# Performance work log

Hardware: AMD Instinct MI355X
Metric: run time of the kernel (lower is better)

## Reference

```python
import jax, jax.numpy as jnp
import numpy as np

B, S, H = 1, 2048, 4096
N_HEADS, N_KV, HEAD_DIM = 32, 8, 128
ROPE_THETA = 10000.0


def setup_inputs() -> dict:
    key = jax.random.key(0)
    k1, k2, k3 = jax.random.split(key, 3)
    hidden_states = jax.random.normal(k1, (B, S, H), dtype=jnp.float32)
    # fused QKV projection weight: rows = (n_heads + 2*n_kv_heads) * head_dim
    Wqkv = jax.random.normal(k2, ((N_HEADS + 2 * N_KV) * HEAD_DIM, H), dtype=jnp.float32) * 0.02
    Wo = jax.random.normal(k3, (H, N_HEADS * HEAD_DIM), dtype=jnp.float32) * 0.02
    return {"hidden_states": hidden_states, "Wqkv": Wqkv, "Wo": Wo}


def _rope_tables(seqlen, dim, theta):
    inv_freq = 1.0 / (theta ** (jnp.arange(0, dim, 2, dtype=jnp.float32) / dim))  # [dim/2]
    t = jnp.arange(seqlen, dtype=jnp.float32)
    freqs = jnp.outer(t, inv_freq)  # [S, dim/2]
    return jnp.cos(freqs), jnp.sin(freqs)


def _apply_rope(x, cos, sin):
    # torch code: reshape(...,2,-1).transpose -> view_as_complex pairs (x[j], x[j+d/2])
    # i.e. NeoX rotate-half on first/second halves of head_dim.
    d2 = x.shape[-1] // 2
    x1, x2 = x[..., :d2], x[..., d2:]
    c = cos[None, :, None, :]  # [1,S,1,d/2]
    s = sin[None, :, None, :]
    return jnp.concatenate([x1 * c - x2 * s, x1 * s + x2 * c], axis=-1)


def reference(hidden_states, Wqkv, Wo):
    b, s, h = hidden_states.shape
    # fused QKV projection
    qkv = jnp.einsum('bsh,oh->bso', hidden_states, Wqkv)
    q_end = N_HEADS * HEAD_DIM
    k_end = q_end + N_KV * HEAD_DIM
    xq = qkv[..., :q_end].reshape(b, s, N_HEADS, HEAD_DIM)
    xk = qkv[..., q_end:k_end].reshape(b, s, N_KV, HEAD_DIM)
    xv = qkv[..., k_end:].reshape(b, s, N_KV, HEAD_DIM)
    # RoPE (start_pos = 0 prefill)
    cos, sin = _rope_tables(s, HEAD_DIM, ROPE_THETA)
    xq = _apply_rope(xq, cos, sin)
    xk = _apply_rope(xk, cos, sin)
    # GQA: expand kv heads to query heads (head h uses kv head h // groups)
    groups = N_HEADS // N_KV
    xk = jnp.repeat(xk, groups, axis=2)  # [b,s,nH,hd]
    xv = jnp.repeat(xv, groups, axis=2)
    # causal attention, softmax scale 1/sqrt(head_dim) (flash_attn default, softcap=0)
    scale = 1.0 / jnp.sqrt(jnp.float32(HEAD_DIM))
    scores = jnp.einsum('bqhd,bkhd->bhqk', xq, xk) * scale
    causal = jnp.tril(jnp.ones((s, s), dtype=bool))
    scores = jnp.where(causal[None, None, :, :], scores, jnp.float32(-1e30))
    probs = jax.nn.softmax(scores, axis=-1)
    out = jnp.einsum('bhqk,bkhd->bqhd', probs, xv).reshape(b, s, N_HEADS * HEAD_DIM)
    attn_output = jnp.einsum('bsd,hd->bsh', out, Wo)
    return attn_output
```

## Files before the change

### kernel.cpp

```cpp
#include <hip/hip_runtime.h>
#include <stdint.h>

typedef unsigned short u16;
typedef unsigned int   u32;
typedef short bf16x8 __attribute__((ext_vector_type(8)));
typedef float f32x4  __attribute__((ext_vector_type(4)));

__device__ __forceinline__ u16 f2bf(float f) {
    union { float f; u32 u; } v; v.f = f;
    u32 u = v.u;
    u32 r = (u + 0x7fffu + ((u >> 16) & 1u)) >> 16;
    return (u16)r;
}
__device__ __forceinline__ float bf2f(u16 h) {
    union { u32 u; float f; } v; v.u = ((u32)h) << 16;
    return v.f;
}

__device__ __forceinline__ void gload_lds16(const void* g, void* l) {
    __builtin_amdgcn_global_load_lds(
        (__attribute__((address_space(1))) void*)g,
        (__attribute__((address_space(3))) void*)l,
        16, 0, 0);
}

__global__ __launch_bounds__(256) void cvt_all(const float4* __restrict__ s1, uint2* __restrict__ d1,
                                               const float4* __restrict__ s2, uint2* __restrict__ d2,
                                               const float4* __restrict__ s3, uint2* __restrict__ d3) {
    const float4* s; uint2* d; int i;
    int b = blockIdx.x;
    if (b < 8192)        { s = s1; d = d1; i = b * 256 + threadIdx.x; }
    else if (b < 32768)  { s = s2; d = d2; i = (b - 8192) * 256 + threadIdx.x; }
    else                 { s = s3; d = d3; i = (b - 32768) * 256 + threadIdx.x; }
    float4 v = s[i];
    uint2 o;
    o.x = (u32)f2bf(v.x) | ((u32)f2bf(v.y) << 16);
    o.y = (u32)f2bf(v.z) | ((u32)f2bf(v.w) << 16);
    d[i] = o;
}

template <typename OUT_T>
__global__ __launch_bounds__(256) void gemm_bt(const u16* __restrict__ A,
                                               const u16* __restrict__ B,
                                               OUT_T* __restrict__ C,
                                               int M, int N, int K) {
    __shared__ u16 As[2][128 * 32];
    __shared__ u16 Bs[2][128 * 32];

    const int tid  = threadIdx.x;
    const int lane = tid & 63;
    const int wv   = tid >> 6;
    const int row0 = blockIdx.y * 128;
    const int col0 = blockIdx.x * 128;

    const int wm = (wv >> 1) * 64;
    const int wn = (wv & 1) * 64;
    const int fr = lane & 15;
    const int fq = (lane >> 4) * 8;

    const int srow = lane >> 2;
    const int scol = (lane & 3) * 8;

    f32x4 acc[4][4];
#pragma unroll
    for (int i = 0; i < 4; ++i)
#pragma unroll
        for (int j = 0; j < 4; ++j) acc[i][j] = f32x4{0.f, 0.f, 0.f, 0.f};

    auto stage = [&](int buf, int k0) {
#pragma unroll
        for (int i = 0; i < 2; ++i) {
            const int chunk = wv * 2 + i;
            const int r     = chunk * 16 + srow;
            gload_lds16(A + (size_t)(row0 + r) * K + k0 + scol, &As[buf][r * 32 + scol]);
            gload_lds16(B + (size_t)(col0 + r) * K + k0 + scol, &Bs[buf][r * 32 + scol]);
        }
    };

    const int nk = K >> 5;
    stage(0, 0);

    for (int ki = 0; ki < nk; ++ki) {
        __syncthreads();
        if (ki + 1 < nk) stage((ki + 1) & 1, (ki + 1) << 5);

        const u16* as = As[ki & 1];
        const u16* bs = Bs[ki & 1];
        bf16x8 af[4], bf[4];
#pragma unroll
        for (int mt = 0; mt < 4; ++mt)
            af[mt] = *(const bf16x8*)&as[(wm + mt * 16 + fr) * 32 + fq];
#pragma unroll
        for (int nt = 0; nt < 4; ++nt)
            bf[nt] = *(const bf16x8*)&bs[(wn + nt * 16 + fr) * 32 + fq];
#pragma unroll
        for (int mt = 0; mt < 4; ++mt)
#pragma unroll
            for (int nt = 0; nt < 4; ++nt)
                acc[mt][nt] = __builtin_amdgcn_mfma_f32_16x16x32_bf16(
                    af[mt], bf[nt], acc[mt][nt], 0, 0, 0);
    }

    const int orow4 = (lane >> 4) * 4;
    const int ocol  = lane & 15;
#pragma unroll
    for (int mt = 0; mt < 4; ++mt)
#pragma unroll
        for (int nt = 0; nt < 4; ++nt)
#pragma unroll
            for (int r = 0; r < 4; ++r) {
                int mm = row0 + wm + mt * 16 + orow4 + r;
                int nn = col0 + wn + nt * 16 + ocol;
                float v = acc[mt][nt][r];
                if constexpr (sizeof(OUT_T) == 2)
                    C[(size_t)mm * N + nn] = (OUT_T)f2bf(v);
                else
                    C[(size_t)mm * N + nn] = (OUT_T)v;
            }
}

__global__ __launch_bounds__(256) void prep_kv(const u16* __restrict__ qkv,
                                               u16* __restrict__ Kb,
                                               u16* __restrict__ Vt) {
    if (blockIdx.x < 4096) {
        int id = blockIdx.x * 256 + threadIdx.x;
        int d  = id & 63;
        int t  = id >> 6;
        int kh = t & 7;
        int s  = t >> 3;
        const size_t rowbase = (size_t)s * 6144 + 4096;
        float inv = __expf(-(float)d * (9.210340371976184f / 64.0f));
        float ang = (float)s * inv;
        float cs, sn; __sincosf(ang, &sn, &cs);
        float x1 = bf2f(qkv[rowbase + kh * 128 + d]);
        float x2 = bf2f(qkv[rowbase + kh * 128 + d + 64]);
        size_t o = ((size_t)kh * 2048 + s) * 128 + d;
        Kb[o]      = f2bf(x1 * cs - x2 * sn);
        Kb[o + 64] = f2bf(x1 * sn + x2 * cs);
    } else {
        int id = (blockIdx.x - 4096) * 256 + threadIdx.x;
        int s8 = id & 255;
        int d  = (id >> 8) & 127;
        int vh = id >> 15;
        u16 tmp[8];
#pragma unroll
        for (int j = 0; j < 8; ++j)
            tmp[j] = qkv[(size_t)(s8 * 8 + j) * 6144 + 5120 + vh * 128 + d];
        *(uint4*)(Vt + ((size_t)vh * 128 + d) * 2048 + s8 * 8) = *(uint4*)tmp;
    }
}

__device__ __forceinline__ void attn_pass(const bf16x8 qf[4], f32x4 acc[8], float lr[4],
                                          const u16* Ks, const u16* Vs, u16* Psw,
                                          int w, int m, int quad, bool diag, float sl2e) {
    f32x4 sacc[4];
#pragma unroll
    for (int nt = 0; nt < 4; ++nt) sacc[nt] = f32x4{0.f, 0.f, 0.f, 0.f};
#pragma unroll
    for (int kk = 0; kk < 4; ++kk) {
#pragma unroll
        for (int nt = 0; nt < 4; ++nt) {
            int pos = (kk * 4 + quad) ^ (m & 7);
            bf16x8 b = *(const bf16x8*)&Ks[(nt * 16 + m) * 128 + pos * 8];
            sacc[nt] = __builtin_amdgcn_mfma_f32_16x16x32_bf16(qf[kk], b, sacc[nt], 0, 0, 0);
        }
    }

#pragma unroll
    for (int nt = 0; nt < 4; ++nt)
#pragma unroll
        for (int r = 0; r < 4; ++r) {
            float p = __builtin_amdgcn_exp2f(sacc[nt][r] * sl2e);
            if (diag && (nt * 16 + m > w * 16 + quad * 4 + r)) p = 0.f;
            sacc[nt][r] = p;
            lr[r] += p;
        }

#pragma unroll
    for (int nt = 0; nt < 4; ++nt)
#pragma unroll
        for (int r = 0; r < 4; ++r)
            Psw[(quad * 4 + r) * 72 + nt * 16 + m] = f2bf(sacc[nt][r]);

#pragma unroll
    for (int kk2 = 0; kk2 < 2; ++kk2) {
        bf16x8 a = *(const bf16x8*)&Psw[m * 72 + kk2 * 32 + quad * 8];
#pragma unroll
        for (int nt = 0; nt < 8; ++nt) {
            int n = nt * 16 + m;
            int pos = (kk2 * 4 + quad) ^ (m & 7);
            bf16x8 b = *(const bf16x8*)&Vs[n * 64 + pos * 8];
            acc[nt] = __builtin_amdgcn_mfma_f32_16x16x32_bf16(a, b, acc[nt], 0, 0, 0);
        }
    }
}

__global__ __launch_bounds__(256) void attn_mfma(const u16* __restrict__ qkv,
                                                 const u16* __restrict__ Kb,
                                                 const u16* __restrict__ Vt,
                                                 u16* __restrict__ ctx) {
    __shared__ u16 Ks[2][64 * 128];
    __shared__ u16 Vs[2][128 * 64];
    __shared__ u16 Ps[4][16 * 72];

    const int tid  = threadIdx.x;
    const int lane = tid & 63;
    const int w    = tid >> 6;
    const int m    = lane & 15;
    const int quad = lane >> 4;
    const int h    = blockIdx.y;
    const int kh   = h >> 2;
    const int qtA  = blockIdx.x;
    const int qtB  = 31 - qtA;

    const u16* Ktile0 = Kb + (size_t)kh * 2048 * 128;
    const u16* Vtile0 = Vt + (size_t)kh * 128 * 2048;
    const float sl2e = 0.08838834764831845f * 1.4426950408889634f;

    auto stage = [&](int buf, int kt) {
        const u16* Kt = Ktile0 + (size_t)kt * 64 * 128;
#pragma unroll
        for (int i = 0; i < 4; ++i) {
            int slot = i * 256 + tid;
            int row = slot >> 4, cp = slot & 15;
            int gc = cp ^ (row & 7);
            gload_lds16(Kt + row * 128 + gc * 8, &Ks[buf][slot * 8]);
        }
        const u16* Vtt = Vtile0 + kt * 64;
#pragma unroll
        for (int i = 0; i < 4; ++i) {
            int slot = i * 256 + tid;
            int row = slot >> 3, cp = slot & 7;
            int gc = cp ^ (row & 7);
            gload_lds16(Vtt + (size_t)row * 2048 + gc * 8, &Vs[buf][slot * 8]);
        }
    };

    bf16x8 qa[4], qb[4];
#pragma unroll
    for (int which = 0; which < 2; ++which) {
        const int qt = which ? qtB : qtA;
        const int s  = qt * 64 + w * 16 + m;
        bf16x8 raw[4];
        const u16* qp = qkv + (size_t)s * 6144 + h * 128 + quad * 8;
#pragma unroll
        for (int kk = 0; kk < 4; ++kk)
            raw[kk] = *(const bf16x8*)(qp + kk * 32);
        bf16x8* dst = which ? qb : qa;
#pragma unroll
        for (int half = 0; half < 2; ++half)
#pragma unroll
            for (int j = 0; j < 8; ++j) {
                int d = half * 32 + quad * 8 + j;
                float inv = __expf(-(float)d * (9.210340371976184f / 64.0f));
                float ang = (float)s * inv;
                float cs, sn; __sincosf(ang, &sn, &cs);
                float x1 = bf2f(((const u16*)&raw[half])[j]);
                float x2 = bf2f(((const u16*)&raw[half + 2])[j]);
                ((u16*)&dst[half])[j]     = f2bf(x1 * cs - x2 * sn);
                ((u16*)&dst[half + 2])[j] = f2bf(x1 * sn + x2 * cs);
            }
    }

    f32x4 accA[8], accB[8];
#pragma unroll
    for (int i = 0; i < 8; ++i) { accA[i] = f32x4{0.f, 0.f, 0.f, 0.f}; accB[i] = f32x4{0.f, 0.f, 0.f, 0.f}; }
    float lA[4] = {0.f, 0.f, 0.f, 0.f};
    float lB[4] = {0.f, 0.f, 0.f, 0.f};

    stage(0, 0);
    for (int kt = 0; kt <= qtB; ++kt) {
        __syncthreads();
        if (kt < qtB) stage((kt + 1) & 1, kt + 1);

        const u16* ks = Ks[kt & 1];
        const u16* vs = Vs[kt & 1];
        if (kt <= qtA)
            attn_pass(qa, accA, lA, ks, vs, Ps[w], w, m, quad, kt == qtA, sl2e);
        attn_pass(qb, accB, lB, ks, vs, Ps[w], w, m, quad, kt == qtB, sl2e);
    }

#pragma unroll
    for (int which = 0; which < 2; ++which) {
        const int qt   = which ? qtB : qtA;
        f32x4*   acc   = which ? accB : accA;
        float*   lr    = which ? lB   : lA;
#pragma unroll
        for (int r = 0; r < 4; ++r) {
            float s_ = lr[r];
            s_ += __shfl_xor(s_, 1);
            s_ += __shfl_xor(s_, 2);
            s_ += __shfl_xor(s_, 4);
            s_ += __shfl_xor(s_, 8);
            lr[r] = s_;
        }
#pragma unroll
        for (int r = 0; r < 4; ++r) {
            float inv = 1.f / lr[r];
            size_t rowg = (size_t)(qt * 64 + w * 16 + quad * 4 + r);
#pragma unroll
            for (int nt = 0; nt < 8; ++nt)
                ctx[rowg * 4096 + h * 128 + nt * 16 + m] = f2bf(acc[nt][r] * inv);
        }
    }
}

extern "C" void kernel_launch(void* const* d_in, const int* in_sizes, int n_in,
                              void* d_out, int out_size, void* d_ws, size_t ws_size,
                              hipStream_t stream) {
    const float* hs   = (const float*)d_in[0];
    const float* wqkv = (const float*)d_in[1];
    const float* wo   = (const float*)d_in[2];
    float* out = (float*)d_out;

    char* ws = (char*)d_ws;
    u16* hA  = (u16*)ws;  ws += (size_t)2048 * 4096 * 2;
    u16* wQ  = (u16*)ws;  ws += (size_t)6144 * 4096 * 2;
    u16* wO  = (u16*)ws;  ws += (size_t)4096 * 4096 * 2;
    u16* qkv = (u16*)ws;  ws += (size_t)2048 * 6144 * 2;
    u16* Kb  = (u16*)ws;  ws += (size_t)8 * 2048 * 128 * 2;
    u16* Vt  = (u16*)ws;  ws += (size_t)8 * 128 * 2048 * 2;
    u16* ctx = (u16*)ws;  ws += (size_t)2048 * 4096 * 2;

    cvt_all<<<49152, 256, 0, stream>>>((const float4*)hs,   (uint2*)hA,
                                       (const float4*)wqkv, (uint2*)wQ,
                                       (const float4*)wo,   (uint2*)wO);

    gemm_bt<u16><<<dim3(48, 16), 256, 0, stream>>>(hA, wQ, qkv, 2048, 6144, 4096);

    prep_kv<<<5120, 256, 0, stream>>>(qkv, Kb, Vt);

    attn_mfma<<<dim3(16, 32), 256, 0, stream>>>(qkv, Kb, Vt, ctx);

    gemm_bt<float><<<dim3(32, 16), 256, 0, stream>>>(ctx, wO, out, 2048, 4096, 4096);
}
```

Baseline: 509.8 us.

## Keep attention probabilities in registers via transposed QK and permlane packing

The QK^T MFMA now computes the transposed score tile (K as A operand), so each lane holds a column of scores. These are packed to bf16 with v_cvt_pk_bf16_f32 and reshuffled with permlane swaps straight into the PV A-operand layout, which removes the per-wave LDS round trip for P. The two query tiles are also interleaved inside one pass to add MFMA independence, s_setprio is raised around the MFMA blocks, and launch bounds now request 2 blocks per SM. The row-sum reduction is reworked to fit the new layout. Risks: higher register pressure from keeping both tiles' scores live, and correctness depends on the exact permlane lane mapping.

New measurement: 505.6 us. No clear change (-0.8%).

```diff
diff --git a/kernel.cpp b/kernel.cpp
--- a/kernel.cpp
+++ b/kernel.cpp
@@ -150,58 +150,84 @@
     }
 }
 
-__device__ __forceinline__ void attn_pass(const bf16x8 qf[4], f32x4 acc[8], float lr[4],
-                                          const u16* Ks, const u16* Vs, u16* Psw,
-                                          int w, int m, int quad, bool diag, float sl2e) {
-    f32x4 sacc[4];
-#pragma unroll
-    for (int nt = 0; nt < 4; ++nt) sacc[nt] = f32x4{0.f, 0.f, 0.f, 0.f};
-#pragma unroll
-    for (int kk = 0; kk < 4; ++kk) {
+__device__ __forceinline__ void softmax_pack(f32x4 s[4], bool diag, int w, int m, int quad,
+                                             float sl2e, float& lsum, bf16x8 af[2]) {
+#pragma unroll
+    for (int nt = 0; nt < 4; ++nt)
+#pragma unroll
+        for (int r = 0; r < 4; ++r) {
+            float p = __builtin_amdgcn_exp2f(s[nt][r] * sl2e);
+            if (diag && (nt * 16 + quad * 4 + r > w * 16 + m)) p = 0.f;
+            s[nt][r] = p;
+            lsum += p;
+        }
+#pragma unroll
+    for (int kk2 = 0; kk2 < 2; ++kk2)
+#pragma unroll
+        for (int ws = 0; ws < 2; ++ws) {
+            u32 a, b;
+            asm("v_cvt_pk_bf16_f32 %0, %1, %2"
+                : "=v"(a) : "v"(s[2 * kk2][2 * ws]), "v"(s[2 * kk2][2 * ws + 1]));
+            asm("v_cvt_pk_bf16_f32 %0, %1, %2"
+                : "=v"(b) : "v"(s[2 * kk2 + 1][2 * ws]), "v"(s[2 * kk2 + 1][2 * ws + 1]));
+            asm("v_permlane32_swap_b32 %0, %1" : "+v"(a), "+v"(b));
+            asm("v_permlane16_swap_b32 %0, %1" : "+v"(a), "+v"(b));
+            ((u32*)&af[kk2])[ws]     = a;
+            ((u32*)&af[kk2])[ws + 2] = b;
+        }
+}
+
+template <bool TWO>
+__device__ __forceinline__ void attn_pass2(const bf16x8 qfA[4], const bf16x8 qfB[4],
+                                           f32x4 accA[8], f32x4 accB[8],
+                                           float& lA, float& lB,
+                                           const u16* Ks, const u16* Vs,
+                                           int w, int m, int quad,
+                                           bool diagA, bool diagB, float sl2e) {
+    f32x4 sA[4], sB[4];
+#pragma unroll
+    for (int nt = 0; nt < 4; ++nt) {
+        sA[nt] = f32x4{0.f, 0.f, 0.f, 0.f};
+        sB[nt] = f32x4{0.f, 0.f, 0.f, 0.f};
+    }
+
+    __builtin_amdgcn_s_setprio(1);
+#pragma unroll
+    for (int kk = 0; kk < 4; ++kk)
 #pragma unroll
         for (int nt = 0; nt < 4; ++nt) {
             int pos = (kk * 4 + quad) ^ (m & 7);
             bf16x8 b = *(const bf16x8*)&Ks[(nt * 16 + m) * 128 + pos * 8];
-            sacc[nt] = __builtin_amdgcn_mfma_f32_16x16x32_bf16(qf[kk], b, sacc[nt], 0, 0, 0);
-        }
-    }
-
-#pragma unroll
-    for (int nt = 0; nt < 4; ++nt)
-#pragma unroll
-        for (int r = 0; r < 4; ++r) {
-            float p = __builtin_amdgcn_exp2f(sacc[nt][r] * sl2e);
-            if (diag && (nt * 16 + m > w * 16 + quad * 4 + r)) p = 0.f;
-            sacc[nt][r] = p;
-            lr[r] += p;
-        }
-
-#pragma unroll
-    for (int nt = 0; nt < 4; ++nt)
-#pragma unroll
-        for (int r = 0; r < 4; ++r)
-            Psw[(quad * 4 + r) * 72 + nt * 16 + m] = f2bf(sacc[nt][r]);
-
-#pragma unroll
-    for (int kk2 = 0; kk2 < 2; ++kk2) {
-        bf16x8 a = *(const bf16x8*)&Psw[m * 72 + kk2 * 32 + quad * 8];
+            sB[nt] = __builtin_amdgcn_mfma_f32_16x16x32_bf16(b, qfB[kk], sB[nt], 0, 0, 0);
+            if constexpr (TWO)
+                sA[nt] = __builtin_amdgcn_mfma_f32_16x16x32_bf16(b, qfA[kk], sA[nt], 0, 0, 0);
+        }
+    __builtin_amdgcn_s_setprio(0);
+
+    bf16x8 afA[2], afB[2];
+    softmax_pack(sB, diagB, w, m, quad, sl2e, lB, afB);
+    if constexpr (TWO) softmax_pack(sA, diagA, w, m, quad, sl2e, lA, afA);
+
+    __builtin_amdgcn_s_setprio(1);
+#pragma unroll
+    for (int kk2 = 0; kk2 < 2; ++kk2)
 #pragma unroll
         for (int nt = 0; nt < 8; ++nt) {
-            int n = nt * 16 + m;
             int pos = (kk2 * 4 + quad) ^ (m & 7);
-            bf16x8 b = *(const bf16x8*)&Vs[n * 64 + pos * 8];
-            acc[nt] = __builtin_amdgcn_mfma_f32_16x16x32_bf16(a, b, acc[nt], 0, 0, 0);
-        }
-    }
-}
-
-__global__ __launch_bounds__(256) void attn_mfma(const u16* __restrict__ qkv,
-                                                 const u16* __restrict__ Kb,
-                                                 const u16* __restrict__ Vt,
-                                                 u16* __restrict__ ctx) {
+            bf16x8 b = *(const bf16x8*)&Vs[(nt * 16 + m) * 64 + pos * 8];
+            accB[nt] = __builtin_amdgcn_mfma_f32_16x16x32_bf16(afB[kk2], b, accB[nt], 0, 0, 0);
+            if constexpr (TWO)
+                accA[nt] = __builtin_amdgcn_mfma_f32_16x16x32_bf16(afA[kk2], b, accA[nt], 0, 0, 0);
+        }
+    __builtin_amdgcn_s_setprio(0);
+}
+
+__global__ __launch_bounds__(256, 2) void attn_mfma(const u16* __restrict__ qkv,
+                                                    const u16* __restrict__ Kb,
+                                                    const u16* __restrict__ Vt,
+                                                    u16* __restrict__ ctx) {
     __shared__ u16 Ks[2][64 * 128];
     __shared__ u16 Vs[2][128 * 64];
-    __shared__ u16 Ps[4][16 * 72];
 
     const int tid  = threadIdx.x;
     const int lane = tid & 63;
@@ -265,8 +291,7 @@
     f32x4 accA[8], accB[8];
 #pragma unroll
     for (int i = 0; i < 8; ++i) { accA[i] = f32x4{0.f, 0.f, 0.f, 0.f}; accB[i] = f32x4{0.f, 0.f, 0.f, 0.f}; }
-    float lA[4] = {0.f, 0.f, 0.f, 0.f};
-    float lB[4] = {0.f, 0.f, 0.f, 0.f};
+    float lA = 0.f, lB = 0.f;
 
     stage(0, 0);
     for (int kt = 0; kt <= qtB; ++kt) {
@@ -276,31 +301,30 @@
         const u16* ks = Ks[kt & 1];
         const u16* vs = Vs[kt & 1];
         if (kt <= qtA)
-            attn_pass(qa, accA, lA, ks, vs, Ps[w], w, m, quad, kt == qtA, sl2e);
-        attn_pass(qb, accB, lB, ks, vs, Ps[w], w, m, quad, kt == qtB, sl2e);
+            attn_pass2<true >(qa, qb, accA, accB, lA, lB, ks, vs, w, m, quad,
+                              kt == qtA, false, sl2e);
+        else
+            attn_pass2<false>(qa, qb, accA, accB, lA, lB, ks, vs, w, m, quad,
+                              false, kt == qtB, sl2e);
     }
 
 #pragma unroll
     for (int which = 0; which < 2; ++which) {
-        const int qt   = which ? qtB : qtA;
-        f32x4*   acc   = which ? accB : accA;
-        float*   lr    = which ? lB   : lA;
+        const int qt  = which ? qtB : qtA;
+        f32x4*   acc  = which ? accB : accA;
+        float    l    = which ? lB   : lA;
+        l += __shfl_xor(l, 16);
+        l += __shfl_xor(l, 32);
+        float linv[4];
+#pragma unroll
+        for (int r = 0; r < 4; ++r)
+            linv[r] = 1.f / __shfl(l, quad * 4 + r);
 #pragma unroll
         for (int r = 0; r < 4; ++r) {
-            float s_ = lr[r];
-            s_ += __shfl_xor(s_, 1);
-            s_ += __shfl_xor(s_, 2);
-            s_ += __shfl_xor(s_, 4);
-            s_ += __shfl_xor(s_, 8);
-            lr[r] = s_;
-        }
-#pragma unroll
-        for (int r = 0; r < 4; ++r) {
-            float inv = 1.f / lr[r];
             size_t rowg = (size_t)(qt * 64 + w * 16 + quad * 4 + r);
 #pragma unroll
             for (int nt = 0; nt < 8; ++nt)
-                ctx[rowg * 4096 + h * 128 + nt * 16 + m] = f2bf(acc[nt][r] * inv);
+                ctx[rowg * 4096 + h * 128 + nt * 16 + m] = f2bf(acc[nt][r] * linv[r]);
         }
     }
 }
```
